# Kernel optimization log

Hardware: AMD Instinct MI355X
Metric: run time of the kernel (lower is better)

Reference implementation:

```python
import jax, jax.numpy as jnp
import numpy as np

B, T, H = 64, 512, 1024

def setup_inputs() -> dict:
    key = jax.random.key(0)
    ks = jax.random.split(key, 6)
    scale = 1.0 / np.sqrt(H)
    return {
        "s_t": jax.random.normal(ks[0], (B, H), dtype=jnp.float32),
        "prev_s": jax.random.normal(ks[1], (B, T, H), dtype=jnp.float32),
        "W_prev": jax.random.normal(ks[2], (H, H), dtype=jnp.float32) * scale,
        "W_s": jax.random.normal(ks[3], (H, H), dtype=jnp.float32) * scale,
        "b_s": jax.random.normal(ks[4], (H,), dtype=jnp.float32) * scale,
        "v": jax.random.normal(ks[5], (H,), dtype=jnp.float32) * scale,
    }

def reference(s_t, prev_s, W_prev, W_s, b_s, v):
    # et = W_prev(prev_s)                       [B,T,H]
    et = jnp.einsum('bth,oh->bto', prev_s, W_prev)
    # dec_fea = W_s(s_t).unsqueeze(1)           [B,1,H]
    dec_fea = (jnp.einsum('bh,oh->bo', s_t, W_s) + b_s)[:, None, :]
    # scores = v(tanh(et + dec_fea)).squeeze    [B,T]
    scores = jnp.einsum('bth,h->bt', jnp.tanh(et + dec_fea), v)
    at = jax.nn.softmax(scores, axis=1)         # [B,T]
    ct_d = jnp.einsum('bt,bth->bh', at, prev_s)  # bmm(at[:,None,:], prev_s).squeeze(1)
    new_prev_s = jnp.concatenate([prev_s, s_t[:, None, :]], axis=1)  # [B,T+1,H]
    return ct_d, new_prev_s
```

## Files before the change

kernel.cpp:

```cpp
#include <hip/hip_runtime.h>
#include <hip/hip_bf16.h>

#define B_DIM 64
#define T_DIM 512
#define H_DIM 1024

typedef __attribute__((ext_vector_type(4))) float f32x4;

#define AQ8_OFF  0UL
#define BQ8_OFF  33554432UL
#define DEC_OFF  34603008UL
#define PART_OFF 34865152UL
#define AT_OFF   35913728UL

__device__ __forceinline__ unsigned cvt4_fp8(float a, float b, float c, float d) {
  unsigned r = 0;
  r = __builtin_amdgcn_cvt_pk_fp8_f32(a, b, r, false);
  r = __builtin_amdgcn_cvt_pk_fp8_f32(c, d, r, true);
  return r;
}

__device__ __forceinline__ void gload_lds16(const void* g, void* l) {
  __builtin_amdgcn_global_load_lds(
      (const __attribute__((address_space(1))) void*)g,
      (__attribute__((address_space(3))) void*)l, 16, 0, 0);
}


__global__ __launch_bounds__(256) void prep_ws(
    const float* __restrict__ prev,
    const float* __restrict__ st,
    const float* __restrict__ Wp,
    const float* __restrict__ Ws,
    const float* __restrict__ bs,
    float* __restrict__ out,
    unsigned char* __restrict__ Aq,
    unsigned char* __restrict__ Wq,
    float* __restrict__ dec) {
  __shared__ unsigned char lq[2][16][528];
  int bid = blockIdx.x;
  int tid = threadIdx.x;

  if (bid < 256) {
    int lane = tid & 63, w = tid >> 6;
    int o = bid * 4 + w;
    const float4* wrow = (const float4*)(Ws + (size_t)o * H_DIM);
    float4 w0 = wrow[lane], w1 = wrow[64 + lane],
           w2 = wrow[128 + lane], w3 = wrow[192 + lane];
    const float4* st4 = (const float4*)st;
    float bias = bs[o];
    #pragma unroll 8
    for (int b = 0; b < B_DIM; b++) {
      const float4* s = st4 + (size_t)b * 256;
      float4 s0 = s[lane], s1 = s[64 + lane], s2 = s[128 + lane], s3 = s[192 + lane];
      float p = w0.x * s0.x + w0.y * s0.y + w0.z * s0.z + w0.w * s0.w
              + w1.x * s1.x + w1.y * s1.y + w1.z * s1.z + w1.w * s1.w
              + w2.x * s2.x + w2.y * s2.y + w2.z * s2.z + w2.w * s2.w
              + w3.x * s3.x + w3.y * s3.y + w3.z * s3.z + w3.w * s3.w;
      p += __shfl_xor(p, 1);  p += __shfl_xor(p, 2);
      p += __shfl_xor(p, 4);  p += __shfl_xor(p, 8);
      p += __shfl_xor(p, 16); p += __shfl_xor(p, 32);
      if (lane == 0) dec[(size_t)b * H_DIM + o] = p + bias;
    }
  } else if (bid < 4352 && ((bid - 256) & 1)) {
    int mt = (bid - 256) >> 1;
    const f32x4* src4 = (const f32x4*)prev + (size_t)mt * 4096;
    int b = mt >> 5, t0 = (mt & 31) * 16;
    f32x4* dst4 = (f32x4*)out + 16384 + (size_t)b * 131328 + (size_t)t0 * 256;
    f32x4 cb[8];
    #pragma unroll
    for (int p = 0; p < 8; p++) cb[p] = src4[p * 256 + tid];
    #pragma unroll
    for (int p = 0; p < 8; p++) dst4[p * 256 + tid] = cb[p];
    #pragma unroll
    for (int p = 0; p < 8; p++) cb[p] = src4[2048 + p * 256 + tid];
    #pragma unroll
    for (int p = 0; p < 8; p++) dst4[2048 + p * 256 + tid] = cb[p];
  } else if (bid < 4416) {
    bool isA = bid < 4352;
    int mt = isA ? ((bid - 256) >> 1) : (bid - 4352);
    const f32x4* src4 = (const f32x4*)(isA ? prev : Wp) + (size_t)mt * 4096;
    unsigned char* q8 = (isA ? Aq : Wq) + (size_t)mt * 16384;
    float scale = isA ? 4.f : 16.f;

    f32x4 buf[8];
    #pragma unroll
    for (int p = 0; p < 8; p++) {
      int idx = p * 256 + tid;
      int r = idx >> 7, cg = idx & 127;
      buf[p] = src4[(size_t)r * 256 + cg];
    }
    #pragma unroll
    for (int p = 0; p < 8; p++) {
      int idx = p * 256 + tid;
      int r = idx >> 7, cg = idx & 127;
      *(unsigned*)&lq[0][r][cg * 4] =
          cvt4_fp8(buf[p][0] * scale, buf[p][1] * scale,
                   buf[p][2] * scale, buf[p][3] * scale);
    }
    #pragma unroll
    for (int p = 0; p < 8; p++) {
      int idx = p * 256 + tid;
      int r = idx >> 7, cg = idx & 127;
      buf[p] = src4[(size_t)r * 256 + 128 + cg];
    }
    asm volatile("s_waitcnt lgkmcnt(0)" ::: "memory");
    __builtin_amdgcn_s_barrier();

    #pragma unroll
    for (int cc = 0; cc < 2; cc++) {
      int c = cc * 256 + tid;
      int ktl = c >> 5, ci = c & 31;
      int r0 = (2 * ci) & 15, oct = ci >> 3;
      uint2 lo = *(const uint2*)&lq[0][r0][ktl * 32 + oct * 8];
      uint2 hi = *(const uint2*)&lq[0][r0 + 1][ktl * 32 + oct * 8];
      uint4 val = make_uint4(lo.x, lo.y, hi.x, hi.y);
      *(uint4*)(q8 + (size_t)ktl * 512 + ci * 16) = val;
    }
    #pragma unroll
    for (int p = 0; p < 8; p++) {
      int idx = p * 256 + tid;
      int r = idx >> 7, cg = idx & 127;
      *(unsigned*)&lq[1][r][cg * 4] =
          cvt4_fp8(buf[p][0] * scale, buf[p][1] * scale,
                   buf[p][2] * scale, buf[p][3] * scale);
    }
    asm volatile("s_waitcnt lgkmcnt(0)" ::: "memory");
    __builtin_amdgcn_s_barrier();

    #pragma unroll
    for (int cc = 0; cc < 2; cc++) {
      int c = cc * 256 + tid;
      int ktl = c >> 5, ci = c & 31;
      int r0 = (2 * ci) & 15, oct = ci >> 3;
      uint2 lo = *(const uint2*)&lq[1][r0][ktl * 32 + oct * 8];
      uint2 hi = *(const uint2*)&lq[1][r0 + 1][ktl * 32 + oct * 8];
      uint4 val = make_uint4(lo.x, lo.y, hi.x, hi.y);
      *(uint4*)(q8 + (size_t)(16 + ktl) * 512 + ci * 16) = val;
    }
  } else {
    const f32x4* s4 = (const f32x4*)st;
    for (int b = 0; b < B_DIM; b++) {
      f32x4* o4 = (f32x4*)out + 16384 + (size_t)b * 131328 + 131072;
      o4[tid] = s4[(size_t)b * 256 + tid];
    }
  }
}

__global__ __launch_bounds__(256, 3) void score_gemm(
    const unsigned char* __restrict__ Aq,
    const unsigned char* __restrict__ Bq,
    const float* __restrict__ dec,
    const float* __restrict__ v,
    float* __restrict__ part)
{
  __shared__ __align__(16) unsigned char ldsA[2][8192];
  __shared__ __align__(16) unsigned char ldsB[2][8192];

  int orig = blockIdx.x;
  int swz = (orig & 7) * 256 + (orig >> 3);
  int bm = swz >> 3, bn = swz & 7;

  int tid = threadIdx.x;
  int lane = tid & 63, w = tid >> 6;
  int wm = w >> 1, wn = w & 1;
  size_t m0 = (size_t)bm * 128;

  f32x4 acc[4][4];
  #pragma unroll
  for (int i = 0; i < 4; i++)
    #pragma unroll
    for (int j = 0; j < 4; j++) {
      f32x4 z; z[0] = 0.f; z[1] = 0.f; z[2] = 0.f; z[3] = 0.f;
      acc[i][j] = z;
    }

  int fA = tid >> 5, cif = tid & 31;
  const unsigned char* aSrc0 =
      Aq + ((size_t)(bm * 8 + (fA >> 1)) * 32 + (fA & 1)) * 512 + (size_t)cif * 16;
  const unsigned char* aSrc1 =
      Aq + ((size_t)(bm * 8 + (fA >> 1) + 4) * 32 + (fA & 1)) * 512 + (size_t)cif * 16;
  const unsigned char* bSrc0 =
      Bq + ((size_t)(bn * 8 + (fA >> 1)) * 32 + (fA & 1)) * 512 + (size_t)cif * 16;
  const unsigned char* bSrc1 =
      Bq + ((size_t)(bn * 8 + (fA >> 1) + 4) * 32 + (fA & 1)) * 512 + (size_t)cif * 16;

#define STAGE(buf, t) do { \
    size_t ko = (size_t)(t) * 1024; \
    gload_lds16(aSrc0 + ko, &ldsA[(buf)][tid * 16]); \
    gload_lds16(aSrc1 + ko, &ldsA[(buf)][tid * 16 + 4096]); \
    gload_lds16(bSrc0 + ko, &ldsB[(buf)][tid * 16]); \
    gload_lds16(bSrc1 + ko, &ldsB[(buf)][tid * 16 + 4096]); \
  } while (0)

  STAGE(0, 0);

  #pragma unroll 2
  for (int t = 0; t < 16; t++) {
    int cur = t & 1, nxt = cur ^ 1;
    if (t < 15) {
      STAGE(nxt, t + 1);
      asm volatile("s_waitcnt vmcnt(4)" ::: "memory");
    } else {
      asm volatile("s_waitcnt vmcnt(0)" ::: "memory");
    }
    __builtin_amdgcn_s_barrier();
    asm volatile("" ::: "memory");

    const unsigned char* Ac = &ldsA[cur][0];
    const unsigned char* Bc = &ldsB[cur][0];
    long av[4][2], bv[4][2];
    #pragma unroll
    for (int mf = 0; mf < 4; mf++)
      #pragma unroll
      for (int kk = 0; kk < 2; kk++)
        av[mf][kk] = *(const long*)(Ac + ((wm * 4 + mf) * 2 + kk) * 512 + lane * 8);
    #pragma unroll
    for (int nf = 0; nf < 4; nf++)
      #pragma unroll
      for (int kk = 0; kk < 2; kk++)
        bv[nf][kk] = *(const long*)(Bc + ((wn * 4 + nf) * 2 + kk) * 512 + lane * 8);

    __builtin_amdgcn_s_setprio(1);
    #pragma unroll
    for (int kk = 0; kk < 2; kk++)
      #pragma unroll
      for (int mf = 0; mf < 4; mf++)
        #pragma unroll
        for (int nf = 0; nf < 4; nf++)
          acc[mf][nf] = __builtin_amdgcn_mfma_f32_16x16x32_fp8_fp8(
              av[mf][kk], bv[nf][kk], acc[mf][nf], 0, 0, 0);
    __builtin_amdgcn_s_setprio(0);
    asm volatile("" ::: "memory");
    __builtin_amdgcn_s_barrier();
  }
#undef STAGE

  int b = (int)(m0 >> 9);
  int lr = lane >> 4, lc = lane & 15;
  int n0 = bn * 128;
  float dv[4], vv[4];
  #pragma unroll
  for (int nf = 0; nf < 4; nf++) {
    int col = n0 + wn * 64 + nf * 16 + lc;
    dv[nf] = dec[(size_t)b * H_DIM + col];
    vv[nf] = v[col];
  }
  float* epi = (float*)&ldsA[0][0];
  #pragma unroll
  for (int mf = 0; mf < 4; mf++) {
    #pragma unroll
    for (int r = 0; r < 4; r++) {
      float s = 0.f;
      #pragma unroll
      for (int nf = 0; nf < 4; nf++) {
        float x = acc[mf][nf][r] * 0.015625f + dv[nf];
        x = fminf(fmaxf(x, -15.f), 15.f);
        float e = __expf(2.f * x);
        s += vv[nf] * (e - 1.f) * __builtin_amdgcn_rcpf(e + 1.f);
      }
      s += __shfl_xor(s, 1); s += __shfl_xor(s, 2);
      s += __shfl_xor(s, 4); s += __shfl_xor(s, 8);
      if (lc == 0) epi[(wm * 64 + mf * 16 + lr * 4 + r) * 2 + wn] = s;
    }
  }
  __syncthreads();
  if (tid < 128) {
    part[(m0 + tid) * 8 + bn] = epi[tid * 2] + epi[tid * 2 + 1];
  }
}

__global__ __launch_bounds__(256) void ctd_ws(
    const unsigned char* __restrict__ Aq,
    const float* __restrict__ part,
    float* __restrict__ out) {
  __shared__ float sc[512];
  __shared__ float red[8];
  __shared__ float at_l[512];
  int blk = blockIdx.x;
  int tid = threadIdx.x;
  int b = blk >> 3;

  #pragma unroll
  for (int rep = 0; rep < 2; rep++) {
    int t = rep * 256 + tid;
    const float* p = part + ((size_t)b * 512 + t) * 8;
    sc[t] = p[0] + p[1] + p[2] + p[3] + p[4] + p[5] + p[6] + p[7];
  }
  __syncthreads();
  float m = fmaxf(sc[tid], sc[tid + 256]);
  for (int d = 1; d < 64; d <<= 1) m = fmaxf(m, __shfl_xor(m, d));
  if ((tid & 63) == 0) red[tid >> 6] = m;
  __syncthreads();
  m = fmaxf(fmaxf(red[0], red[1]), fmaxf(red[2], red[3]));
  float e0 = __expf(sc[tid] - m), e1 = __expf(sc[tid + 256] - m);
  float s = e0 + e1;
  for (int d = 1; d < 64; d <<= 1) s += __shfl_xor(s, d);
  if ((tid & 63) == 0) red[4 + (tid >> 6)] = s;
  __syncthreads();
  s = red[4] + red[5] + red[6] + red[7];
  float inv = 1.f / s;
  at_l[tid] = e0 * inv;
  at_l[tid + 256] = e1 * inv;
  __syncthreads();

  int lane = tid & 63, w = tid >> 6;
  int kt = (blk & 7) * 4 + w;
  int lc = lane & 15, lr = lane >> 4;
  float a8[8] = {0.f, 0.f, 0.f, 0.f, 0.f, 0.f, 0.f, 0.f};
  const unsigned char* base =
      Aq + ((size_t)b * 1024 + kt) * 512 + (size_t)lane * 8;
  #pragma unroll 8
  for (int mt = 0; mt < 32; mt++) {
    float a = at_l[mt * 16 + lc];
    uint2 uv = *(const uint2*)(base + (size_t)mt * 16384);
    a8[0] += a * __builtin_amdgcn_cvt_f32_fp8(uv.x, 0);
    a8[1] += a * __builtin_amdgcn_cvt_f32_fp8(uv.x, 1);
    a8[2] += a * __builtin_amdgcn_cvt_f32_fp8(uv.x, 2);
    a8[3] += a * __builtin_amdgcn_cvt_f32_fp8(uv.x, 3);
    a8[4] += a * __builtin_amdgcn_cvt_f32_fp8(uv.y, 0);
    a8[5] += a * __builtin_amdgcn_cvt_f32_fp8(uv.y, 1);
    a8[6] += a * __builtin_amdgcn_cvt_f32_fp8(uv.y, 2);
    a8[7] += a * __builtin_amdgcn_cvt_f32_fp8(uv.y, 3);
  }
  #pragma unroll
  for (int d = 1; d < 16; d <<= 1)
    #pragma unroll
    for (int j = 0; j < 8; j++) a8[j] += __shfl_xor(a8[j], d);
  if (lc == 0) {
    #pragma unroll
    for (int j = 0; j < 8; j++)
      out[(size_t)b * H_DIM + kt * 32 + lr * 8 + j] = a8[j] * 0.25f;
  }
}

extern "C" void kernel_launch(void* const* d_in, const int* in_sizes, int n_in,
                              void* d_out, int out_size, void* d_ws, size_t ws_size,
                              hipStream_t stream) {
  (void)in_sizes; (void)n_in; (void)out_size; (void)ws_size;
  const float* s_t    = (const float*)d_in[0];
  const float* prev_s = (const float*)d_in[1];
  const float* W_prev = (const float*)d_in[2];
  const float* W_s    = (const float*)d_in[3];
  const float* b_s    = (const float*)d_in[4];
  const float* v      = (const float*)d_in[5];
  float* out = (float*)d_out;
  char* ws = (char*)d_ws;

  unsigned char* Aq = (unsigned char*)(ws + AQ8_OFF);
  unsigned char* Wq = (unsigned char*)(ws + BQ8_OFF);
  float* dec  = (float*)(ws + DEC_OFF);
  float* part = (float*)(ws + PART_OFF);

  prep_ws<<<4417, 256, 0, stream>>>(prev_s, s_t, W_prev, W_s, b_s, out, Aq, Wq, dec);
  score_gemm<<<2048, 256, 0, stream>>>(Aq, Wq, dec, v, part);
  ctd_ws<<<512, 256, 0, stream>>>(Aq, part, out);
}
```

Baseline: 148.0 us.

## Fuse prev_s copy into FP8 quantization blocks and simplify LDS repack

Previously each 16-row tile of prev_s was read twice: once by a copy block writing it into the concatenated output, and once by a quantization block. Now one block loads the tile once, writes the fp32 copy and quantizes it to FP8. Each wave handles its own 256-column slice and repacks through a per-wave LDS buffer without block barriers. This halves prev_s global reads and the block count, at the cost of more registers per thread and a changed FP8 packing granularity (uint2 stores), which must still match the layout score_gemm expects.

```diff
diff --git a/kernel.cpp b/kernel.cpp
--- a/kernel.cpp
+++ b/kernel.cpp
@@ -11,7 +11,6 @@
 #define BQ8_OFF  33554432UL
 #define DEC_OFF  34603008UL
 #define PART_OFF 34865152UL
-#define AT_OFF   35913728UL
 
 __device__ __forceinline__ unsigned cvt4_fp8(float a, float b, float c, float d) {
   unsigned r = 0;
@@ -37,12 +36,12 @@
     unsigned char* __restrict__ Aq,
     unsigned char* __restrict__ Wq,
     float* __restrict__ dec) {
-  __shared__ unsigned char lq[2][16][528];
+  __shared__ unsigned char lq[4][16][264];
   int bid = blockIdx.x;
   int tid = threadIdx.x;
+  int lane = tid & 63, w = tid >> 6;
 
   if (bid < 256) {
-    int lane = tid & 63, w = tid >> 6;
     int o = bid * 4 + w;
     const float4* wrow = (const float4*)(Ws + (size_t)o * H_DIM);
     float4 w0 = wrow[lane], w1 = wrow[64 + lane],
@@ -62,81 +61,35 @@
       p += __shfl_xor(p, 16); p += __shfl_xor(p, 32);
       if (lane == 0) dec[(size_t)b * H_DIM + o] = p + bias;
     }
-  } else if (bid < 4352 && ((bid - 256) & 1)) {
-    int mt = (bid - 256) >> 1;
-    const f32x4* src4 = (const f32x4*)prev + (size_t)mt * 4096;
-    int b = mt >> 5, t0 = (mt & 31) * 16;
-    f32x4* dst4 = (f32x4*)out + 16384 + (size_t)b * 131328 + (size_t)t0 * 256;
-    f32x4 cb[8];
-    #pragma unroll
-    for (int p = 0; p < 8; p++) cb[p] = src4[p * 256 + tid];
-    #pragma unroll
-    for (int p = 0; p < 8; p++) dst4[p * 256 + tid] = cb[p];
-    #pragma unroll
-    for (int p = 0; p < 8; p++) cb[p] = src4[2048 + p * 256 + tid];
-    #pragma unroll
-    for (int p = 0; p < 8; p++) dst4[2048 + p * 256 + tid] = cb[p];
-  } else if (bid < 4416) {
-    bool isA = bid < 4352;
-    int mt = isA ? ((bid - 256) >> 1) : (bid - 4352);
+  } else if (bid < 2368) {
+    bool isA = bid < 2304;
+    int mt = isA ? bid - 256 : bid - 2304;
     const f32x4* src4 = (const f32x4*)(isA ? prev : Wp) + (size_t)mt * 4096;
+    f32x4* dst4 = nullptr;
+    if (isA) {
+      int b = mt >> 5, t0 = (mt & 31) * 16;
+      dst4 = (f32x4*)out + 16384 + (size_t)b * 131328 + (size_t)t0 * 256;
+    }
     unsigned char* q8 = (isA ? Aq : Wq) + (size_t)mt * 16384;
     float scale = isA ? 4.f : 16.f;
 
-    f32x4 buf[8];
-    #pragma unroll
-    for (int p = 0; p < 8; p++) {
-      int idx = p * 256 + tid;
-      int r = idx >> 7, cg = idx & 127;
-      buf[p] = src4[(size_t)r * 256 + cg];
-    }
-    #pragma unroll
-    for (int p = 0; p < 8; p++) {
-      int idx = p * 256 + tid;
-      int r = idx >> 7, cg = idx & 127;
-      *(unsigned*)&lq[0][r][cg * 4] =
-          cvt4_fp8(buf[p][0] * scale, buf[p][1] * scale,
-                   buf[p][2] * scale, buf[p][3] * scale);
-    }
-    #pragma unroll
-    for (int p = 0; p < 8; p++) {
-      int idx = p * 256 + tid;
-      int r = idx >> 7, cg = idx & 127;
-      buf[p] = src4[(size_t)r * 256 + 128 + cg];
+    f32x4 buf[16];
+    #pragma unroll
+    for (int r = 0; r < 16; r++)
+      buf[r] = src4[(size_t)r * 256 + w * 64 + lane];
+    #pragma unroll
+    for (int r = 0; r < 16; r++) {
+      if (isA) dst4[(size_t)r * 256 + w * 64 + lane] = buf[r];
+      *(unsigned*)&lq[w][r][lane * 4] =
+          cvt4_fp8(buf[r][0] * scale, buf[r][1] * scale,
+                   buf[r][2] * scale, buf[r][3] * scale);
     }
     asm volatile("s_waitcnt lgkmcnt(0)" ::: "memory");
-    __builtin_amdgcn_s_barrier();
-
-    #pragma unroll
-    for (int cc = 0; cc < 2; cc++) {
-      int c = cc * 256 + tid;
-      int ktl = c >> 5, ci = c & 31;
-      int r0 = (2 * ci) & 15, oct = ci >> 3;
-      uint2 lo = *(const uint2*)&lq[0][r0][ktl * 32 + oct * 8];
-      uint2 hi = *(const uint2*)&lq[0][r0 + 1][ktl * 32 + oct * 8];
-      uint4 val = make_uint4(lo.x, lo.y, hi.x, hi.y);
-      *(uint4*)(q8 + (size_t)ktl * 512 + ci * 16) = val;
-    }
-    #pragma unroll
-    for (int p = 0; p < 8; p++) {
-      int idx = p * 256 + tid;
-      int r = idx >> 7, cg = idx & 127;
-      *(unsigned*)&lq[1][r][cg * 4] =
-          cvt4_fp8(buf[p][0] * scale, buf[p][1] * scale,
-                   buf[p][2] * scale, buf[p][3] * scale);
-    }
-    asm volatile("s_waitcnt lgkmcnt(0)" ::: "memory");
-    __builtin_amdgcn_s_barrier();
-
-    #pragma unroll
-    for (int cc = 0; cc < 2; cc++) {
-      int c = cc * 256 + tid;
-      int ktl = c >> 5, ci = c & 31;
-      int r0 = (2 * ci) & 15, oct = ci >> 3;
-      uint2 lo = *(const uint2*)&lq[1][r0][ktl * 32 + oct * 8];
-      uint2 hi = *(const uint2*)&lq[1][r0 + 1][ktl * 32 + oct * 8];
-      uint4 val = make_uint4(lo.x, lo.y, hi.x, hi.y);
-      *(uint4*)(q8 + (size_t)(16 + ktl) * 512 + ci * 16) = val;
+
+    #pragma unroll
+    for (int f = 0; f < 8; f++) {
+      uint2 val = *(const uint2*)&lq[w][lane & 15][f * 32 + (lane >> 4) * 8];
+      *(uint2*)(q8 + (size_t)(w * 8 + f) * 512 + lane * 8) = val;
     }
   } else {
     const f32x4* s4 = (const f32x4*)st;
@@ -352,7 +305,7 @@
   float* dec  = (float*)(ws + DEC_OFF);
   float* part = (float*)(ws + PART_OFF);
 
-  prep_ws<<<4417, 256, 0, stream>>>(prev_s, s_t, W_prev, W_s, b_s, out, Aq, Wq, dec);
+  prep_ws<<<2369, 256, 0, stream>>>(prev_s, s_t, W_prev, W_s, b_s, out, Aq, Wq, dec);
   score_gemm<<<2048, 256, 0, stream>>>(Aq, Wq, dec, v, part);
   ctd_ws<<<512, 256, 0, stream>>>(Aq, part, out);
 }
```

Measured after the change: 134.6 us, median of 2. -9.0%, faster.
